# Kernel tuning notes

Hardware: AMD Instinct MI355X
Metric: run time of the kernel (lower is better)

The kernel has to match this reference:

```python
import math
import jax, jax.numpy as jnp
import numpy as np

D = 1024        # latent_dim
H = 16          # num latent heads
HD = D // H     # head dim = 64
T_EMB = 9       # max(diffusion_steps+1, 2)
CLIP = 1.0      # latent_update_clip
LN_EPS = 1e-5


def layer_norm(x, g, b):
    m = jnp.mean(x, axis=-1, keepdims=True)
    v = jnp.mean(jnp.square(x - m), axis=-1, keepdims=True)
    return (x - m) * jax.lax.rsqrt(v + LN_EPS) * g + b


def setup_inputs() -> dict:
    key = jax.random.key(0)
    ks = jax.random.split(key, 10)
    B, S = 64, 64
    s = 0.02
    return {
        "latents": jax.random.normal(ks[0], (B, S, D), jnp.float32),
        "t_table": jax.random.normal(ks[1], (T_EMB, D), jnp.float32) * s,
        "attn_g": jnp.ones((D,), jnp.float32),
        "attn_b": jnp.zeros((D,), jnp.float32),
        "ffn_g": jnp.ones((D,), jnp.float32),
        "ffn_b": jnp.zeros((D,), jnp.float32),
        "Wq": jax.random.normal(ks[2], (D, D), jnp.float32) * s,
        "Wk": jax.random.normal(ks[3], (D, D), jnp.float32) * s,
        "Wv": jax.random.normal(ks[4], (D, D), jnp.float32) * s,
        "Wo": jax.random.normal(ks[5], (D, D), jnp.float32) * s,
        "Win": jax.random.normal(ks[6], (2 * D, D), jnp.float32) * s,
        "b_in": jnp.zeros((2 * D,), jnp.float32),
        "Wout": jax.random.normal(ks[7], (D, 2 * D), jnp.float32) * s,
        "b_out": jnp.zeros((D,), jnp.float32),
        "steps": 8,
    }


def _slot_attention(x, Wq, Wk, Wv, Wo):
    B, S, _ = x.shape
    scale = 1.0 / math.sqrt(HD)
    # torch Linear: y = x @ W.T ; weights stored (out, in)
    q = (x @ Wq.T).reshape(B, S, H, HD)
    k = (x @ Wk.T).reshape(B, S, H, HD)
    v = (x @ Wv.T).reshape(B, S, H, HD)
    scores = jnp.einsum("bqhd,bkhd->bhqk", q, k) * scale
    probs = jax.nn.softmax(scores, axis=-1)
    out = jnp.einsum("bhqk,bkhd->bqhd", probs, v).reshape(B, S, D)
    return out @ Wo.T


def reference(latents, t_table, attn_g, attn_b, ffn_g, ffn_b,
              Wq, Wk, Wv, Wo, Win, b_in, Wout, b_out, steps):
    h = latents
    for step in range(steps):
        step_id = min(step, T_EMB - 1)
        t_emb = t_table[step_id][None, None, :]          # [1,1,D]
        attn_update = _slot_attention(layer_norm(h + t_emb, attn_g, attn_b),
                                      Wq, Wk, Wv, Wo)
        ffn_in = layer_norm(h + t_emb + attn_update, ffn_g, ffn_b)
        ffn_update = jax.nn.silu(ffn_in @ Win.T + b_in) @ Wout.T + b_out
        update = attn_update + ffn_update
        unorm = jnp.maximum(jnp.linalg.norm(update, axis=-1, keepdims=True), 1e-6)
        update = update * jnp.minimum(CLIP / unorm, 1.0)
        h = h + update / steps
    return h
```

## Files before the change

kernel.cpp:

```cpp
#include <hip/hip_runtime.h>
#include <hip/hip_bf16.h>

typedef __attribute__((ext_vector_type(8))) short bf16x8;
typedef __attribute__((ext_vector_type(4))) float f32x4;
typedef __attribute__((ext_vector_type(4))) int i32x4;

static __device__ __forceinline__ short f2bf(float f) {
    __hip_bfloat16 h = __float2bfloat16(f);
    return __builtin_bit_cast(short, h);
}

static __device__ __forceinline__ void gload_lds16(const short* g, short* l) {
    __builtin_amdgcn_global_load_lds((const __attribute__((address_space(1))) void*)g,
                                     (__attribute__((address_space(3))) void*)l, 16, 0, 0);
}

__global__ void convert_kernel(const float* __restrict__ src, short* __restrict__ dst, int n) {
    for (int i = blockIdx.x * blockDim.x + threadIdx.x; i < n; i += gridDim.x * blockDim.x)
        dst[i] = f2bf(src[i]);
}

__global__ void copy_kernel(const float* __restrict__ src, float* __restrict__ dst, int n) {
    for (int i = blockIdx.x * blockDim.x + threadIdx.x; i < n; i += gridDim.x * blockDim.x)
        dst[i] = src[i];
}

__global__ __launch_bounds__(256) void ln_kernel(
    const float* __restrict__ hsrc, const float* __restrict__ trow,
    const float* __restrict__ add,
    const float* __restrict__ g, const float* __restrict__ bb,
    short* __restrict__ out)
{
    const int row = blockIdx.x;
    const int tid = threadIdx.x;
    const int lane = tid & 63;
    const int wid = tid >> 6;
    __shared__ float red[4];
    const float* hr = hsrc + (size_t)row * 1024;
    float x[4];
    float s = 0.f;
    #pragma unroll
    for (int i = 0; i < 4; ++i) {
        int c = tid + i * 256;
        float v = hr[c] + trow[c];
        if (add) v += add[(size_t)row * 1024 + c];
        x[i] = v; s += v;
    }
    #pragma unroll
    for (int o = 32; o >= 1; o >>= 1) s += __shfl_xor(s, o, 64);
    if (lane == 0) red[wid] = s;
    __syncthreads();
    float mean = (red[0] + red[1] + red[2] + red[3]) * (1.0f / 1024.0f);
    __syncthreads();
    float s2 = 0.f;
    #pragma unroll
    for (int i = 0; i < 4; ++i) { float d = x[i] - mean; s2 += d * d; }
    #pragma unroll
    for (int o = 32; o >= 1; o >>= 1) s2 += __shfl_xor(s2, o, 64);
    if (lane == 0) red[wid] = s2;
    __syncthreads();
    float var = (red[0] + red[1] + red[2] + red[3]) * (1.0f / 1024.0f);
    float rstd = rsqrtf(var + 1e-5f);
    #pragma unroll
    for (int i = 0; i < 4; ++i) {
        int c = tid + i * 256;
        out[(size_t)row * 1024 + c] = f2bf((x[i] - mean) * rstd * g[c] + bb[c]);
    }
}

__global__ __launch_bounds__(256) void clipln_kernel(
    const float* __restrict__ upd, float* __restrict__ h,
    const float* __restrict__ trow,
    const float* __restrict__ g, const float* __restrict__ bb,
    short* __restrict__ out)
{
    const int row = blockIdx.x;
    const int tid = threadIdx.x;
    const int lane = tid & 63;
    const int wid = tid >> 6;
    __shared__ float red[4];
    const float* ur = upd + (size_t)row * 1024;
    float u[4], hn[4];
    float s = 0.f;
    #pragma unroll
    for (int i = 0; i < 4; ++i) { u[i] = ur[tid + i * 256]; s += u[i] * u[i]; }
    #pragma unroll
    for (int o = 32; o >= 1; o >>= 1) s += __shfl_xor(s, o, 64);
    if (lane == 0) red[wid] = s;
    __syncthreads();
    float nrm = sqrtf(red[0] + red[1] + red[2] + red[3]);
    float scale = fminf(1.0f / fmaxf(nrm, 1e-6f), 1.0f) * 0.125f;
    __syncthreads();
    float sm = 0.f;
    #pragma unroll
    for (int i = 0; i < 4; ++i) {
        int c = tid + i * 256;
        hn[i] = h[(size_t)row * 1024 + c] + u[i] * scale;
        h[(size_t)row * 1024 + c] = hn[i];
        hn[i] += trow[c];
        sm += hn[i];
    }
    #pragma unroll
    for (int o = 32; o >= 1; o >>= 1) sm += __shfl_xor(sm, o, 64);
    if (lane == 0) red[wid] = sm;
    __syncthreads();
    float mean = (red[0] + red[1] + red[2] + red[3]) * (1.0f / 1024.0f);
    __syncthreads();
    float s2 = 0.f;
    #pragma unroll
    for (int i = 0; i < 4; ++i) { float d = hn[i] - mean; s2 += d * d; }
    #pragma unroll
    for (int o = 32; o >= 1; o >>= 1) s2 += __shfl_xor(s2, o, 64);
    if (lane == 0) red[wid] = s2;
    __syncthreads();
    float var = (red[0] + red[1] + red[2] + red[3]) * (1.0f / 1024.0f);
    float rstd = rsqrtf(var + 1e-5f);
    #pragma unroll
    for (int i = 0; i < 4; ++i) {
        int c = tid + i * 256;
        out[(size_t)row * 1024 + c] = f2bf((hn[i] - mean) * rstd * g[c] + bb[c]);
    }
}

template<int BM, int ACT, int ADD, int BIAS, int OUT_BF16>
__global__ __launch_bounds__(256) void gemm_kernel(
    const short* __restrict__ A, const short* __restrict__ B,
    const float* __restrict__ bias, const float* __restrict__ addsrc,
    void* __restrict__ Cout, int M, int N, int K)
{
    const int bn = blockIdx.x * 128;
    const int bm = blockIdx.y * BM;
    __shared__ __align__(16) short As[2][BM * 64];
    __shared__ __align__(16) short Bs[2][128 * 64];
    const int tid = threadIdx.x;
    const int lane = tid & 63;
    const int wid = tid >> 6;
    const int l15 = lane & 15;
    const int l4 = lane >> 4;

    constexpr int ALOADS = BM / 32;
    constexpr int LOADS = ALOADS + 4;
    constexpr int NF = (BM == 128) ? 4 : 2;
    const int rowbase = (BM == 128) ? (wid >> 1) * 64 : 0;
    const int colbase = (BM == 128) ? (wid & 1) * 64 : wid * 32;

    f32x4 acc[4][NF];
    #pragma unroll
    for (int m = 0; m < 4; ++m)
        #pragma unroll
        for (int n = 0; n < NF; ++n)
            acc[m][n] = (f32x4)(0.f);

    auto stage = [&](int k0, int buf) {
        #pragma unroll
        for (int i = 0; i < ALOADS; ++i) {
            int slot = i * 256 + tid;
            int row = slot >> 3;
            int colb = (slot & 7) * 16;
            int swz = (row & 7) << 4;
            const short* g = A + (size_t)(bm + row) * K + k0 + ((colb ^ swz) >> 1);
            gload_lds16(g, (short*)((char*)As[buf] + slot * 16));
        }
        #pragma unroll
        for (int i = 0; i < 4; ++i) {
            int slot = i * 256 + tid;
            int row = slot >> 3;
            int colb = (slot & 7) * 16;
            int swz = (row & 7) << 4;
            const short* g = B + (size_t)(bn + row) * K + k0 + ((colb ^ swz) >> 1);
            gload_lds16(g, (short*)((char*)Bs[buf] + slot * 16));
        }
    };

    stage(0, 0);
    const int nt = K >> 6;
    for (int t = 0; t < nt; ++t) {
        const int cur = t & 1;
        if (t + 1 < nt) {
            stage((t + 1) << 6, cur ^ 1);
            if constexpr (LOADS == 8) asm volatile("s_waitcnt vmcnt(8)" ::: "memory");
            else                      asm volatile("s_waitcnt vmcnt(6)" ::: "memory");
        } else {
            asm volatile("s_waitcnt vmcnt(0)" ::: "memory");
        }
        __builtin_amdgcn_s_barrier();
        #pragma unroll
        for (int ks = 0; ks < 2; ++ks) {
            int kb = ks * 64 + l4 * 16;
            bf16x8 a[4], b[NF];
            #pragma unroll
            for (int m = 0; m < 4; ++m) {
                int row = rowbase + m * 16 + l15;
                a[m] = *(const bf16x8*)((const char*)As[cur] + row * 128 + (kb ^ ((row & 7) << 4)));
            }
            #pragma unroll
            for (int n = 0; n < NF; ++n) {
                int row = colbase + n * 16 + l15;
                b[n] = *(const bf16x8*)((const char*)Bs[cur] + row * 128 + (kb ^ ((row & 7) << 4)));
            }
            #pragma unroll
            for (int m = 0; m < 4; ++m)
                #pragma unroll
                for (int n = 0; n < NF; ++n)
                    acc[m][n] = __builtin_amdgcn_mfma_f32_16x16x32_bf16(a[m], b[n], acc[m][n], 0, 0, 0);
        }
        __builtin_amdgcn_s_barrier();
    }

    #pragma unroll
    for (int m = 0; m < 4; ++m) {
        int row = bm + rowbase + m * 16 + l4 * 4;
        #pragma unroll
        for (int n = 0; n < NF; ++n) {
            int col = bn + colbase + n * 16 + l15;
            float bv = BIAS ? bias[col] : 0.f;
            #pragma unroll
            for (int r = 0; r < 4; ++r) {
                float v = acc[m][n][r] + bv;
                if (ACT) v = v / (1.f + __expf(-v));
                if (ADD) v += addsrc[(size_t)(row + r) * N + col];
                if (OUT_BF16) ((short*)Cout)[(size_t)(row + r) * N + col] = f2bf(v);
                else          ((float*)Cout)[(size_t)(row + r) * N + col] = v;
            }
        }
    }
}

__global__ __launch_bounds__(256) void attn_kernel(
    const short* __restrict__ qkv,
    short* __restrict__ ctx)
{
    const int blk = blockIdx.x;
    const int b = blk >> 4, hh = blk & 15;
    const int bs0 = b * 64;
    __shared__ __align__(16) short qs[64 * 64];
    __shared__ __align__(16) short ks_[64 * 64];
    __shared__ __align__(16) short vt[64 * 64];
    __shared__ __align__(16) short ps[64 * 64];
    const int tid = threadIdx.x;
    const int lane = tid & 63;
    const int wid = tid >> 6;
    const int l15 = lane & 15;
    const int l4 = lane >> 4;

    #pragma unroll
    for (int i = 0; i < 2; ++i) {
        int slot = i * 256 + tid;
        int row = slot >> 3;
        int colb = (slot & 7) * 16;
        int swz = (row & 7) << 4;
        const short* gq = qkv + (size_t)(bs0 + row) * 3072 + hh * 64 + (slot & 7) * 8;
        *(i32x4*)((char*)qs + row * 128 + (colb ^ swz)) = *(const i32x4*)gq;
        const short* gk = qkv + (size_t)(bs0 + row) * 3072 + 1024 + hh * 64 + (slot & 7) * 8;
        *(i32x4*)((char*)ks_ + row * 128 + (colb ^ swz)) = *(const i32x4*)gk;
        const short* gv = qkv + (size_t)(bs0 + row) * 3072 + 2048 + hh * 64 + (slot & 7) * 8;
        i32x4 vv = *(const i32x4*)gv;
        const short* ve = (const short*)&vv;
        #pragma unroll
        for (int j = 0; j < 8; ++j) {
            int d = (slot & 7) * 8 + j;
            *(short*)((char*)vt + d * 128 + ((row * 2) ^ ((d & 7) << 4))) = ve[j];
        }
    }
    __syncthreads();

    f32x4 sc[4];
    #pragma unroll
    for (int n = 0; n < 4; ++n) sc[n] = (f32x4)(0.f);
    #pragma unroll
    for (int ksz = 0; ksz < 2; ++ksz) {
        int kb = ksz * 64 + l4 * 16;
        int arow = wid * 16 + l15;
        bf16x8 af = *(const bf16x8*)((const char*)qs + arow * 128 + (kb ^ ((arow & 7) << 4)));
        #pragma unroll
        for (int n = 0; n < 4; ++n) {
            int brow = n * 16 + l15;
            bf16x8 bf = *(const bf16x8*)((const char*)ks_ + brow * 128 + (kb ^ ((brow & 7) << 4)));
            sc[n] = __builtin_amdgcn_mfma_f32_16x16x32_bf16(af, bf, sc[n], 0, 0, 0);
        }
    }
    float sm[4];
    #pragma unroll
    for (int r = 0; r < 4; ++r) {
        float m = -1e30f;
        #pragma unroll
        for (int n = 0; n < 4; ++n) { sc[n][r] *= 0.125f; m = fmaxf(m, sc[n][r]); }
        #pragma unroll
        for (int o = 1; o < 16; o <<= 1) m = fmaxf(m, __shfl_xor(m, o, 64));
        float s = 0.f;
        #pragma unroll
        for (int n = 0; n < 4; ++n) { sc[n][r] = __expf(sc[n][r] - m); s += sc[n][r]; }
        #pragma unroll
        for (int o = 1; o < 16; o <<= 1) s += __shfl_xor(s, o, 64);
        sm[r] = 1.f / s;
    }
    #pragma unroll
    for (int n = 0; n < 4; ++n)
        #pragma unroll
        for (int r = 0; r < 4; ++r) {
            int row = wid * 16 + l4 * 4 + r;
            int col = n * 16 + l15;
            *(short*)((char*)ps + row * 128 + ((col * 2) ^ ((row & 7) << 4))) = f2bf(sc[n][r] * sm[r]);
        }
    __syncthreads();

    f32x4 o[4];
    #pragma unroll
    for (int n = 0; n < 4; ++n) o[n] = (f32x4)(0.f);
    #pragma unroll
    for (int ksz = 0; ksz < 2; ++ksz) {
        int kb = ksz * 64 + l4 * 16;
        int arow = wid * 16 + l15;
        bf16x8 af = *(const bf16x8*)((const char*)ps + arow * 128 + (kb ^ ((arow & 7) << 4)));
        #pragma unroll
        for (int n = 0; n < 4; ++n) {
            int vrow = n * 16 + l15;
            bf16x8 bf = *(const bf16x8*)((const char*)vt + vrow * 128 + (kb ^ ((vrow & 7) << 4)));
            o[n] = __builtin_amdgcn_mfma_f32_16x16x32_bf16(af, bf, o[n], 0, 0, 0);
        }
    }
    #pragma unroll
    for (int n = 0; n < 4; ++n)
        #pragma unroll
        for (int r = 0; r < 4; ++r) {
            int row = wid * 16 + l4 * 4 + r;
            int col = n * 16 + l15;
            ctx[(size_t)(bs0 + row) * 1024 + hh * 64 + col] = f2bf(o[n][r]);
        }
}

__global__ __launch_bounds__(256) void clip_kernel(const float* __restrict__ upd, float* __restrict__ h) {
    const int row = blockIdx.x;
    const int tid = threadIdx.x;
    const int lane = tid & 63;
    const int wid = tid >> 6;
    __shared__ float red[4];
    const float* ur = upd + (size_t)row * 1024;
    float x[4];
    float s = 0.f;
    #pragma unroll
    for (int i = 0; i < 4; ++i) { x[i] = ur[tid + i * 256]; s += x[i] * x[i]; }
    #pragma unroll
    for (int o = 32; o >= 1; o >>= 1) s += __shfl_xor(s, o, 64);
    if (lane == 0) red[wid] = s;
    __syncthreads();
    float nrm = sqrtf(red[0] + red[1] + red[2] + red[3]);
    float unorm = fmaxf(nrm, 1e-6f);
    float scale = fminf(1.0f / unorm, 1.0f) * 0.125f;
    #pragma unroll
    for (int i = 0; i < 4; ++i) {
        int c = tid + i * 256;
        h[(size_t)row * 1024 + c] += x[i] * scale;
    }
}

extern "C" void kernel_launch(void* const* d_in, const int* in_sizes, int n_in,
                              void* d_out, int out_size, void* d_ws, size_t ws_size,
                              hipStream_t stream) {
    const float* latents = (const float*)d_in[0];
    const float* t_table = (const float*)d_in[1];
    const float* attn_g  = (const float*)d_in[2];
    const float* attn_b  = (const float*)d_in[3];
    const float* ffn_g   = (const float*)d_in[4];
    const float* ffn_b   = (const float*)d_in[5];
    const float* Wq      = (const float*)d_in[6];
    const float* Wk      = (const float*)d_in[7];
    const float* Wv      = (const float*)d_in[8];
    const float* Wo      = (const float*)d_in[9];
    const float* Win     = (const float*)d_in[10];
    const float* b_in    = (const float*)d_in[11];
    const float* Wout    = (const float*)d_in[12];
    const float* b_out   = (const float*)d_in[13];

    char* ws = (char*)d_ws;
    size_t off = 0;
    auto alloc = [&](size_t bytes) { char* p = ws + off; off += (bytes + 255) & ~(size_t)255; return p; };
    short* wQKV = (short*)alloc((size_t)3072 * 1024 * 2);
    short* wO   = (short*)alloc((size_t)1024 * 1024 * 2);
    short* wIn  = (short*)alloc((size_t)2048 * 1024 * 2);
    short* wOut = (short*)alloc((size_t)1024 * 2048 * 2);
    short* xln  = (short*)alloc((size_t)4096 * 1024 * 2);
    short* qkv  = (short*)alloc((size_t)4096 * 3072 * 2);
    short* hidden = qkv;
    short* ctx  = (short*)alloc((size_t)4096 * 1024 * 2);
    float* au   = (float*)alloc((size_t)4096 * 1024 * 4);
    float* upd  = (float*)alloc((size_t)4096 * 1024 * 4);

    float* h = (float*)d_out;

    convert_kernel<<<1024, 256, 0, stream>>>(Wq,   wQKV,               1024 * 1024);
    convert_kernel<<<1024, 256, 0, stream>>>(Wk,   wQKV + 1024 * 1024, 1024 * 1024);
    convert_kernel<<<1024, 256, 0, stream>>>(Wv,   wQKV + 2048 * 1024, 1024 * 1024);
    convert_kernel<<<1024, 256, 0, stream>>>(Wo,   wO,                 1024 * 1024);
    convert_kernel<<<2048, 256, 0, stream>>>(Win,  wIn,                2048 * 1024);
    convert_kernel<<<2048, 256, 0, stream>>>(Wout, wOut,               2048 * 1024);
    copy_kernel<<<2048, 256, 0, stream>>>(latents, h, 4096 * 1024);

    ln_kernel<<<4096, 256, 0, stream>>>(h, t_table, nullptr, attn_g, attn_b, xln);

    for (int step = 0; step < 8; ++step) {
        const float* trow = t_table + (size_t)step * 1024;
        gemm_kernel<128, 0, 0, 0, 1><<<dim3(24, 32), 256, 0, stream>>>(xln, wQKV, nullptr, nullptr, qkv, 4096, 3072, 1024);
        attn_kernel<<<1024, 256, 0, stream>>>(qkv, ctx);
        gemm_kernel<64, 0, 0, 0, 0><<<dim3(8, 64), 256, 0, stream>>>(ctx, wO, nullptr, nullptr, au, 4096, 1024, 1024);
        ln_kernel<<<4096, 256, 0, stream>>>(h, trow, au, ffn_g, ffn_b, xln);
        gemm_kernel<128, 1, 0, 1, 1><<<dim3(16, 32), 256, 0, stream>>>(xln, wIn, b_in, nullptr, hidden, 4096, 2048, 1024);
        gemm_kernel<64, 0, 1, 1, 0><<<dim3(8, 64), 256, 0, stream>>>(hidden, wOut, b_out, au, upd, 4096, 1024, 2048);
        if (step < 7) {
            clipln_kernel<<<4096, 256, 0, stream>>>(upd, h, t_table + (size_t)(step + 1) * 1024,
                                                    attn_g, attn_b, xln);
        } else {
            clip_kernel<<<4096, 256, 0, stream>>>(upd, h);
        }
    }
}
```

Before: 1.170 ms.

## Use 512-thread GEMM blocks, bf16 intermediates, and XCD-aware tile swizzle

The GEMM kernel moves from 256 to 512 threads per block, so each wave computes a smaller 2xNF fragment tile and the staging loads are spread across more threads. Block IDs are remapped so consecutive tiles are spread across the eight XCDs for better L2 locality. The attention-output and update buffers become bf16 instead of fp32, which halves their memory traffic in the GEMM epilogues and the LN/clip kernels. The cost is lower precision on the residual update path and fewer accumulators per wave, which may reduce MFMA reuse per LDS read.

Result: faster. 1.049 ms (-10.3%).

```diff
diff --git a/kernel.cpp b/kernel.cpp
--- a/kernel.cpp
+++ b/kernel.cpp
@@ -9,6 +9,10 @@
     __hip_bfloat16 h = __float2bfloat16(f);
     return __builtin_bit_cast(short, h);
 }
+static __device__ __forceinline__ float bf2f(short s) {
+    unsigned u = ((unsigned)(unsigned short)s) << 16;
+    return __builtin_bit_cast(float, u);
+}
 
 static __device__ __forceinline__ void gload_lds16(const short* g, short* l) {
     __builtin_amdgcn_global_load_lds((const __attribute__((address_space(1))) void*)g,
@@ -27,7 +31,7 @@
 
 __global__ __launch_bounds__(256) void ln_kernel(
     const float* __restrict__ hsrc, const float* __restrict__ trow,
-    const float* __restrict__ add,
+    const short* __restrict__ add,
     const float* __restrict__ g, const float* __restrict__ bb,
     short* __restrict__ out)
 {
@@ -43,7 +47,7 @@
     for (int i = 0; i < 4; ++i) {
         int c = tid + i * 256;
         float v = hr[c] + trow[c];
-        if (add) v += add[(size_t)row * 1024 + c];
+        if (add) v += bf2f(add[(size_t)row * 1024 + c]);
         x[i] = v; s += v;
     }
     #pragma unroll
@@ -69,7 +73,7 @@
 }
 
 __global__ __launch_bounds__(256) void clipln_kernel(
-    const float* __restrict__ upd, float* __restrict__ h,
+    const short* __restrict__ upd, float* __restrict__ h,
     const float* __restrict__ trow,
     const float* __restrict__ g, const float* __restrict__ bb,
     short* __restrict__ out)
@@ -79,11 +83,11 @@
     const int lane = tid & 63;
     const int wid = tid >> 6;
     __shared__ float red[4];
-    const float* ur = upd + (size_t)row * 1024;
+    const short* ur = upd + (size_t)row * 1024;
     float u[4], hn[4];
     float s = 0.f;
     #pragma unroll
-    for (int i = 0; i < 4; ++i) { u[i] = ur[tid + i * 256]; s += u[i] * u[i]; }
+    for (int i = 0; i < 4; ++i) { u[i] = bf2f(ur[tid + i * 256]); s += u[i] * u[i]; }
     #pragma unroll
     for (int o = 32; o >= 1; o >>= 1) s += __shfl_xor(s, o, 64);
     if (lane == 0) red[wid] = s;
@@ -122,14 +126,18 @@
     }
 }
 
-template<int BM, int ACT, int ADD, int BIAS, int OUT_BF16>
-__global__ __launch_bounds__(256) void gemm_kernel(
+template<int BM, int ACT, int ADD, int BIAS>
+__global__ __launch_bounds__(512) void gemm_kernel(
     const short* __restrict__ A, const short* __restrict__ B,
-    const float* __restrict__ bias, const float* __restrict__ addsrc,
-    void* __restrict__ Cout, int M, int N, int K)
+    const float* __restrict__ bias, const short* __restrict__ addsrc,
+    short* __restrict__ Cout, int M, int N, int K)
 {
-    const int bn = blockIdx.x * 128;
-    const int bm = blockIdx.y * BM;
+    const int nwg = gridDim.x * gridDim.y;
+    const int orig = blockIdx.y * gridDim.x + blockIdx.x;
+    const int swzid = (orig & 7) * (nwg >> 3) + (orig >> 3);
+    const int bn = (swzid % gridDim.x) * 128;
+    const int bm = (swzid / gridDim.x) * BM;
+
     __shared__ __align__(16) short As[2][BM * 64];
     __shared__ __align__(16) short Bs[2][128 * 64];
     const int tid = threadIdx.x;
@@ -138,15 +146,17 @@
     const int l15 = lane & 15;
     const int l4 = lane >> 4;
 
-    constexpr int ALOADS = BM / 32;
-    constexpr int LOADS = ALOADS + 4;
+    constexpr int MF = 2;
     constexpr int NF = (BM == 128) ? 4 : 2;
-    const int rowbase = (BM == 128) ? (wid >> 1) * 64 : 0;
-    const int colbase = (BM == 128) ? (wid & 1) * 64 : wid * 32;
-
-    f32x4 acc[4][NF];
-    #pragma unroll
-    for (int m = 0; m < 4; ++m)
+    const int rowbase = (BM == 128) ? (wid >> 1) * 32 : (wid >> 2) * 32;
+    const int colbase = (BM == 128) ? (wid & 1) * 64 : (wid & 3) * 32;
+
+    constexpr int ALOADS = BM * 8 / 512;
+    constexpr int LOADS = ALOADS + 2;
+
+    f32x4 acc[MF][NF];
+    #pragma unroll
+    for (int m = 0; m < MF; ++m)
         #pragma unroll
         for (int n = 0; n < NF; ++n)
             acc[m][n] = (f32x4)(0.f);
@@ -154,7 +164,7 @@
     auto stage = [&](int k0, int buf) {
         #pragma unroll
         for (int i = 0; i < ALOADS; ++i) {
-            int slot = i * 256 + tid;
+            int slot = i * 512 + tid;
             int row = slot >> 3;
             int colb = (slot & 7) * 16;
             int swz = (row & 7) << 4;
@@ -162,8 +172,8 @@
             gload_lds16(g, (short*)((char*)As[buf] + slot * 16));
         }
         #pragma unroll
-        for (int i = 0; i < 4; ++i) {
-            int slot = i * 256 + tid;
+        for (int i = 0; i < 2; ++i) {
+            int slot = i * 512 + tid;
             int row = slot >> 3;
             int colb = (slot & 7) * 16;
             int swz = (row & 7) << 4;
@@ -178,8 +188,8 @@
         const int cur = t & 1;
         if (t + 1 < nt) {
             stage((t + 1) << 6, cur ^ 1);
-            if constexpr (LOADS == 8) asm volatile("s_waitcnt vmcnt(8)" ::: "memory");
-            else                      asm volatile("s_waitcnt vmcnt(6)" ::: "memory");
+            if constexpr (LOADS == 4) asm volatile("s_waitcnt vmcnt(4)" ::: "memory");
+            else                      asm volatile("s_waitcnt vmcnt(3)" ::: "memory");
         } else {
             asm volatile("s_waitcnt vmcnt(0)" ::: "memory");
         }
@@ -187,9 +197,9 @@
         #pragma unroll
         for (int ks = 0; ks < 2; ++ks) {
             int kb = ks * 64 + l4 * 16;
-            bf16x8 a[4], b[NF];
+            bf16x8 a[MF], b[NF];
             #pragma unroll
-            for (int m = 0; m < 4; ++m) {
+            for (int m = 0; m < MF; ++m) {
                 int row = rowbase + m * 16 + l15;
                 a[m] = *(const bf16x8*)((const char*)As[cur] + row * 128 + (kb ^ ((row & 7) << 4)));
             }
@@ -199,7 +209,7 @@
                 b[n] = *(const bf16x8*)((const char*)Bs[cur] + row * 128 + (kb ^ ((row & 7) << 4)));
             }
             #pragma unroll
-            for (int m = 0; m < 4; ++m)
+            for (int m = 0; m < MF; ++m)
                 #pragma unroll
                 for (int n = 0; n < NF; ++n)
                     acc[m][n] = __builtin_amdgcn_mfma_f32_16x16x32_bf16(a[m], b[n], acc[m][n], 0, 0, 0);
@@ -208,7 +218,7 @@
     }
 
     #pragma unroll
-    for (int m = 0; m < 4; ++m) {
+    for (int m = 0; m < MF; ++m) {
         int row = bm + rowbase + m * 16 + l4 * 4;
         #pragma unroll
         for (int n = 0; n < NF; ++n) {
@@ -218,9 +228,8 @@
             for (int r = 0; r < 4; ++r) {
                 float v = acc[m][n][r] + bv;
                 if (ACT) v = v / (1.f + __expf(-v));
-                if (ADD) v += addsrc[(size_t)(row + r) * N + col];
-                if (OUT_BF16) ((short*)Cout)[(size_t)(row + r) * N + col] = f2bf(v);
-                else          ((float*)Cout)[(size_t)(row + r) * N + col] = v;
+                if (ADD) v += bf2f(addsrc[(size_t)(row + r) * N + col]);
+                Cout[(size_t)(row + r) * N + col] = f2bf(v);
             }
         }
     }
@@ -329,17 +338,17 @@
         }
 }
 
-__global__ __launch_bounds__(256) void clip_kernel(const float* __restrict__ upd, float* __restrict__ h) {
+__global__ __launch_bounds__(256) void clip_kernel(const short* __restrict__ upd, float* __restrict__ h) {
     const int row = blockIdx.x;
     const int tid = threadIdx.x;
     const int lane = tid & 63;
     const int wid = tid >> 6;
     __shared__ float red[4];
-    const float* ur = upd + (size_t)row * 1024;
+    const short* ur = upd + (size_t)row * 1024;
     float x[4];
     float s = 0.f;
     #pragma unroll
-    for (int i = 0; i < 4; ++i) { x[i] = ur[tid + i * 256]; s += x[i] * x[i]; }
+    for (int i = 0; i < 4; ++i) { x[i] = bf2f(ur[tid + i * 256]); s += x[i] * x[i]; }
     #pragma unroll
     for (int o = 32; o >= 1; o >>= 1) s += __shfl_xor(s, o, 64);
     if (lane == 0) red[wid] = s;
@@ -383,8 +392,8 @@
     short* qkv  = (short*)alloc((size_t)4096 * 3072 * 2);
     short* hidden = qkv;
     short* ctx  = (short*)alloc((size_t)4096 * 1024 * 2);
-    float* au   = (float*)alloc((size_t)4096 * 1024 * 4);
-    float* upd  = (float*)alloc((size_t)4096 * 1024 * 4);
+    short* au   = (short*)alloc((size_t)4096 * 1024 * 2);
+    short* upd  = (short*)alloc((size_t)4096 * 1024 * 2);
 
     float* h = (float*)d_out;
 
@@ -400,12 +409,12 @@
 
     for (int step = 0; step < 8; ++step) {
         const float* trow = t_table + (size_t)step * 1024;
-        gemm_kernel<128, 0, 0, 0, 1><<<dim3(24, 32), 256, 0, stream>>>(xln, wQKV, nullptr, nullptr, qkv, 4096, 3072, 1024);
+        gemm_kernel<128, 0, 0, 0><<<dim3(24, 32), 512, 0, stream>>>(xln, wQKV, nullptr, nullptr, qkv, 4096, 3072, 1024);
         attn_kernel<<<1024, 256, 0, stream>>>(qkv, ctx);
-        gemm_kernel<64, 0, 0, 0, 0><<<dim3(8, 64), 256, 0, stream>>>(ctx, wO, nullptr, nullptr, au, 4096, 1024, 1024);
+        gemm_kernel<64, 0, 0, 0><<<dim3(8, 64), 512, 0, stream>>>(ctx, wO, nullptr, nullptr, au, 4096, 1024, 1024);
         ln_kernel<<<4096, 256, 0, stream>>>(h, trow, au, ffn_g, ffn_b, xln);
-        gemm_kernel<128, 1, 0, 1, 1><<<dim3(16, 32), 256, 0, stream>>>(xln, wIn, b_in, nullptr, hidden, 4096, 2048, 1024);
-        gemm_kernel<64, 0, 1, 1, 0><<<dim3(8, 64), 256, 0, stream>>>(hidden, wOut, b_out, au, upd, 4096, 1024, 2048);
+        gemm_kernel<128, 1, 0, 1><<<dim3(16, 32), 512, 0, stream>>>(xln, wIn, b_in, nullptr, hidden, 4096, 2048, 1024);
+        gemm_kernel<64, 0, 1, 1><<<dim3(8, 64), 512, 0, stream>>>(hidden, wOut, b_out, au, upd, 4096, 1024, 2048);
         if (step < 7) {
             clipln_kernel<<<4096, 256, 0, stream>>>(upd, h, t_table + (size_t)(step + 1) * 1024,
                                                     attn_g, attn_b, xln);
```
